# Optimization experiments

Measured on AMD Instinct MI355X. Metric: run time of the kernel, lower is better.

## Reference

```python
import jax, jax.numpy as jnp
import numpy as np


def channel_attention(x):
    # Faithful to torch: proj_key = x.view(B, -1, C) is a memory RESHAPE, not a transpose.
    B, C, H, W = x.shape
    N = H * W
    pq = x.reshape(B, C, N)          # [B, C, N]
    pk = x.reshape(B, N, C)          # [B, N, C] -- reshape, NOT pq transposed
    attn = jax.nn.softmax(jnp.einsum('bcn,bnd->bcd', pq, pk), axis=-1)  # [B, C, C]
    out = jnp.einsum('bcd,bdn->bcn', attn, pq).reshape(B, C, H, W)
    return out + x


def positional_attention(x):
    B, C, H, W = x.shape
    N = H * W
    pk = x.reshape(B, C, N)                                  # [B, C, N]
    # proj_query = pk transposed -> attn[b, n, m] over spatial positions
    attn = jax.nn.softmax(jnp.einsum('bcn,bcm->bnm', pk, pk), axis=-1)  # [B, N, N]
    # out = bmm(pk, attn^T): out[b, c, m] = sum_n pk[b, c, n] * attn[b, m, n]
    out = jnp.einsum('bcn,bmn->bcm', pk, attn).reshape(B, C, H, W)
    return out + x


def setup_inputs() -> dict:
    key = jax.random.key(0)
    x = jax.random.normal(key, (4, 512, 64, 64), dtype=jnp.float32)
    return {"x": x}


def reference(x):
    x_ca = channel_attention(x)
    x_pa = positional_attention(x_ca)
    return x_pa
```

## Files before the change

kernel.cpp:

```cpp
#include <hip/hip_runtime.h>

#define BATCH 4
#define CH 512
#define NSP 4096

typedef __attribute__((ext_vector_type(8))) short bfrag8;
typedef __attribute__((ext_vector_type(4))) float f32x4;
typedef unsigned short u16;

#define AS1 __attribute__((address_space(1)))
#define AS3 __attribute__((address_space(3)))
__device__ __forceinline__ void gload16(const void* g, void* l) {
    __builtin_amdgcn_global_load_lds((const AS1 void*)g, (AS3 void*)l, 16, 0, 0);
}

__device__ __forceinline__ void split_bf16(float y, u16& h, u16& l) {
    unsigned int u = __float_as_uint(y);
    h = (u16)(u >> 16);
    float r = y - __uint_as_float(((unsigned int)h) << 16);
    l = (u16)(__float_as_uint(r) >> 16);
}
__device__ __forceinline__ float join_bf16(u16 h, u16 l) {
    return __uint_as_float(((unsigned int)h) << 16) + __uint_as_float(((unsigned int)l) << 16);
}

__global__ __launch_bounds__(256) void k_prep_cn(const float* __restrict__ X,
                                                 u16* __restrict__ XHi,
                                                 u16* __restrict__ XLo,
                                                 u16* __restrict__ XT1hi,
                                                 u16* __restrict__ XT1lo) {
    __shared__ unsigned int t[64][65];
    const size_t boff = (size_t)blockIdx.z * CH * NSP;
    const int c0 = blockIdx.y * 64, n0 = blockIdx.x * 64;
    const int r = threadIdx.x >> 4, col4 = (threadIdx.x & 15) * 4;
#pragma unroll
    for (int it = 0; it < 4; it++) {
        int rl = r + it * 16;
        float4 v = *(const float4*)(X + boff + (size_t)(c0 + rl) * NSP + n0 + col4);
        ushort4 h, l;
        split_bf16(v.x, h.x, l.x);
        split_bf16(v.y, h.y, l.y);
        split_bf16(v.z, h.z, l.z);
        split_bf16(v.w, h.w, l.w);
        *(ushort4*)(XHi + boff + (size_t)(c0 + rl) * NSP + n0 + col4) = h;
        *(ushort4*)(XLo + boff + (size_t)(c0 + rl) * NSP + n0 + col4) = l;
        t[rl][col4 + 0] = ((unsigned int)h.x << 16) | l.x;
        t[rl][col4 + 1] = ((unsigned int)h.y << 16) | l.y;
        t[rl][col4 + 2] = ((unsigned int)h.z << 16) | l.z;
        t[rl][col4 + 3] = ((unsigned int)h.w << 16) | l.w;
    }
    __syncthreads();
#pragma unroll
    for (int it = 0; it < 4; it++) {
        int cl = r + it * 16;
        unsigned int p0 = t[col4 + 0][cl];
        unsigned int p1 = t[col4 + 1][cl];
        unsigned int p2 = t[col4 + 2][cl];
        unsigned int p3 = t[col4 + 3][cl];
        ushort4 hv, lv;
        hv.x = p0 >> 16; hv.y = p1 >> 16; hv.z = p2 >> 16; hv.w = p3 >> 16;
        lv.x = p0 & 0xffff; lv.y = p1 & 0xffff; lv.z = p2 & 0xffff; lv.w = p3 & 0xffff;
        *(ushort4*)(XT1hi + boff + (size_t)(n0 + cl) * CH + c0 + col4) = hv;
        *(ushort4*)(XT1lo + boff + (size_t)(n0 + cl) * CH + c0 + col4) = lv;
    }
}

__global__ __launch_bounds__(256) void k_prep_nc(const float* __restrict__ X,
                                                 u16* __restrict__ XT2hi,
                                                 u16* __restrict__ XT2lo) {
    __shared__ unsigned int t[64][65];
    const size_t boff = (size_t)blockIdx.z * CH * NSP;
    const int n0 = blockIdx.x * 64, d0 = blockIdx.y * 64;
    const int r = threadIdx.x >> 4, col4 = (threadIdx.x & 15) * 4;
#pragma unroll
    for (int it = 0; it < 4; it++) {
        int rl = r + it * 16;
        float4 v = *(const float4*)(X + boff + (size_t)(n0 + rl) * CH + d0 + col4);
        ushort4 h, l;
        split_bf16(v.x, h.x, l.x);
        split_bf16(v.y, h.y, l.y);
        split_bf16(v.z, h.z, l.z);
        split_bf16(v.w, h.w, l.w);
        t[rl][col4 + 0] = ((unsigned int)h.x << 16) | l.x;
        t[rl][col4 + 1] = ((unsigned int)h.y << 16) | l.y;
        t[rl][col4 + 2] = ((unsigned int)h.z << 16) | l.z;
        t[rl][col4 + 3] = ((unsigned int)h.w << 16) | l.w;
    }
    __syncthreads();
#pragma unroll
    for (int it = 0; it < 4; it++) {
        int cl = r + it * 16;
        unsigned int p0 = t[col4 + 0][cl];
        unsigned int p1 = t[col4 + 1][cl];
        unsigned int p2 = t[col4 + 2][cl];
        unsigned int p3 = t[col4 + 3][cl];
        ushort4 hv, lv;
        hv.x = p0 >> 16; hv.y = p1 >> 16; hv.z = p2 >> 16; hv.w = p3 >> 16;
        lv.x = p0 & 0xffff; lv.y = p1 & 0xffff; lv.z = p2 & 0xffff; lv.w = p3 & 0xffff;
        *(ushort4*)(XT2hi + boff + (size_t)(d0 + cl) * NSP + n0 + col4) = hv;
        *(ushort4*)(XT2lo + boff + (size_t)(d0 + cl) * NSP + n0 + col4) = lv;
    }
}

__global__ __launch_bounds__(256, 2) void k1_mfma(const u16* __restrict__ XHi,
                                                  const u16* __restrict__ XLo,
                                                  const u16* __restrict__ XT2hi,
                                                  const u16* __restrict__ XT2lo,
                                                  float* __restrict__ Pk) {
    __shared__ __align__(16) char smem[32768];
    char* Ahi = smem;
    char* Alo = smem + 8192;
    char* Bhi = smem + 16384;
    char* Blo = smem + 24576;
    const int bid = blockIdx.x;
    const int xcd = bid & 7;
    const int i1 = bid >> 3;
    const int group = xcd * 4 + (i1 >> 4);
    const int b = group >> 3, kz = group & 7;
    const int tile = i1 & 15;
    const int c0 = (tile >> 2) * 128, d0 = (tile & 3) * 128;
    const size_t boff = (size_t)b * CH * NSP;
    const int tid = threadIdx.x, lane = tid & 63, w = tid >> 6;
    const int wr = w >> 1, wc = w & 1;
    const int rl = lane >> 2;
    const int cb = (lane & 3) * 8;
    f32x4 acc[4][4];
#pragma unroll
    for (int i = 0; i < 4; i++)
#pragma unroll
        for (int j = 0; j < 4; j++) acc[i][j] = (f32x4){0.f, 0.f, 0.f, 0.f};

    const int kbeg = kz * 512, kend = kbeg + 512;
    for (int k0 = kbeg; k0 < kend; k0 += 32) {
#pragma unroll
        for (int s = 0; s < 2; s++) {
            int idx = w * 2 + s;
            int row = 16 * idx + rl;
            gload16(XHi + boff + (size_t)(c0 + row) * NSP + k0 + cb, Ahi + idx * 1024);
            gload16(XLo + boff + (size_t)(c0 + row) * NSP + k0 + cb, Alo + idx * 1024);
            gload16(XT2hi + boff + (size_t)(d0 + row) * NSP + k0 + cb, Bhi + idx * 1024);
            gload16(XT2lo + boff + (size_t)(d0 + row) * NSP + k0 + cb, Blo + idx * 1024);
        }
        __syncthreads();
        bfrag8 ah[4], al[4], bh[4], bl[4];
        const int q16 = (lane >> 4) * 16;
        const int l15 = (lane & 15);
#pragma unroll
        for (int i = 0; i < 4; i++) {
            int offa = (wr * 64 + i * 16 + l15) * 64 + q16;
            ah[i] = *(const bfrag8*)(Ahi + offa);
            al[i] = *(const bfrag8*)(Alo + offa);
            int offb = (wc * 64 + i * 16 + l15) * 64 + q16;
            bh[i] = *(const bfrag8*)(Bhi + offb);
            bl[i] = *(const bfrag8*)(Blo + offb);
        }
#pragma unroll
        for (int i = 0; i < 4; i++)
#pragma unroll
            for (int j = 0; j < 4; j++) {
                acc[i][j] = __builtin_amdgcn_mfma_f32_16x16x32_bf16(ah[i], bh[j], acc[i][j], 0, 0, 0);
                acc[i][j] = __builtin_amdgcn_mfma_f32_16x16x32_bf16(ah[i], bl[j], acc[i][j], 0, 0, 0);
                acc[i][j] = __builtin_amdgcn_mfma_f32_16x16x32_bf16(al[i], bh[j], acc[i][j], 0, 0, 0);
            }
        __syncthreads();
    }
    float* Lb = Pk + (size_t)kz * BATCH * CH * CH + (size_t)b * CH * CH;
    const int col = lane & 15, qr = (lane >> 4) * 4;
#pragma unroll
    for (int i = 0; i < 4; i++)
#pragma unroll
        for (int j = 0; j < 4; j++)
#pragma unroll
            for (int r = 0; r < 4; r++)
                Lb[(size_t)(c0 + wr * 64 + 16 * i + qr + r) * CH + d0 + wc * 64 + 16 * j + col] =
                    acc[i][j][r];
}

__global__ __launch_bounds__(256) void k_combine8(const float* __restrict__ Pk,
                                                  float* __restrict__ Lg) {
    const size_t MM = (size_t)BATCH * CH * CH;
    size_t i = ((size_t)blockIdx.x * 256 + threadIdx.x) * 4;
    float4 s = *(const float4*)(Pk + i);
#pragma unroll
    for (int z = 1; z < 8; z++) {
        float4 v = *(const float4*)(Pk + z * MM + i);
        s.x += v.x; s.y += v.y; s.z += v.z; s.w += v.w;
    }
    *(float4*)(Lg + i) = s;
}

__global__ __launch_bounds__(256) void k_softmax_pack512(float* __restrict__ Lg) {
    __shared__ float buf[512];
    __shared__ float red[256];
    const int tid = threadIdx.x;
    float* row = Lg + (size_t)blockIdx.x * 512;
    float2 v = *(const float2*)(row + tid * 2);
    buf[tid * 2] = v.x;
    buf[tid * 2 + 1] = v.y;
    red[tid] = fmaxf(v.x, v.y);
    __syncthreads();
    for (int s = 128; s > 0; s >>= 1) {
        if (tid < s) red[tid] = fmaxf(red[tid], red[tid + s]);
        __syncthreads();
    }
    float m = red[0];
    __syncthreads();
    float e0 = __expf(buf[tid * 2] - m), e1 = __expf(buf[tid * 2 + 1] - m);
    buf[tid * 2] = e0;
    buf[tid * 2 + 1] = e1;
    red[tid] = e0 + e1;
    __syncthreads();
    for (int s = 128; s > 0; s >>= 1) {
        if (tid < s) red[tid] += red[tid + s];
        __syncthreads();
    }
    float inv = 1.0f / red[0];
    u16* u = (u16*)row;
    u16 h0, l0, h1, l1;
    split_bf16(buf[tid * 2] * inv, h0, l0);
    split_bf16(buf[tid * 2 + 1] * inv, h1, l1);
    __syncthreads();
    u[tid * 2] = h0;
    u[tid * 2 + 1] = h1;
    u[512 + tid * 2] = l0;
    u[512 + tid * 2 + 1] = l1;
}

__global__ __launch_bounds__(256, 2) void k3_mfma(const u16* __restrict__ Lu,
                                                  const u16* __restrict__ XT1hi,
                                                  const u16* __restrict__ XT1lo,
                                                  const float* __restrict__ X,
                                                  u16* __restrict__ Yhi,
                                                  u16* __restrict__ Ylo,
                                                  u16* __restrict__ YThi,
                                                  u16* __restrict__ YTlo) {
    __shared__ __align__(16) char smem[33280];
    char* Ahi = smem;
    char* Alo = smem + 8192;
    char* Bhi = smem + 16384;
    char* Blo = smem + 24576;
    const int b = blockIdx.z;
    const u16* Au = Lu + (size_t)b * CH * 1024;
    const size_t boff = (size_t)b * CH * NSP;
    const float* Xb = X + boff;
    const int tid = threadIdx.x, lane = tid & 63, w = tid >> 6;
    const int wr = w >> 1, wc = w & 1;
    const int c0 = blockIdx.y * 128, n0 = blockIdx.x * 128;
    const int rl = lane >> 2;
    const int cb = (lane & 3) * 8;
    f32x4 acc[4][4];
#pragma unroll
    for (int i = 0; i < 4; i++)
#pragma unroll
        for (int j = 0; j < 4; j++) acc[i][j] = (f32x4){0.f, 0.f, 0.f, 0.f};

    for (int k0 = 0; k0 < CH; k0 += 32) {
#pragma unroll
        for (int s = 0; s < 2; s++) {
            int idx = w * 2 + s;
            int row = 16 * idx + rl;
            gload16(Au + (size_t)(c0 + row) * 1024 + k0 + cb, Ahi + idx * 1024);
            gload16(Au + (size_t)(c0 + row) * 1024 + 512 + k0 + cb, Alo + idx * 1024);
            gload16(XT1hi + boff + (size_t)(n0 + row) * CH + k0 + cb, Bhi + idx * 1024);
            gload16(XT1lo + boff + (size_t)(n0 + row) * CH + k0 + cb, Blo + idx * 1024);
        }
        __syncthreads();
        bfrag8 ah[4], al[4], bh[4], bl[4];
        const int q16 = (lane >> 4) * 16;
        const int l15 = (lane & 15);
#pragma unroll
        for (int i = 0; i < 4; i++) {
            int offa = (wr * 64 + i * 16 + l15) * 64 + q16;
            ah[i] = *(const bfrag8*)(Ahi + offa);
            al[i] = *(const bfrag8*)(Alo + offa);
            int offb = (wc * 64 + i * 16 + l15) * 64 + q16;
            bh[i] = *(const bfrag8*)(Bhi + offb);
            bl[i] = *(const bfrag8*)(Blo + offb);
        }
#pragma unroll
        for (int i = 0; i < 4; i++)
#pragma unroll
            for (int j = 0; j < 4; j++) {
                acc[i][j] = __builtin_amdgcn_mfma_f32_16x16x32_bf16(ah[i], bh[j], acc[i][j], 0, 0, 0);
                acc[i][j] = __builtin_amdgcn_mfma_f32_16x16x32_bf16(ah[i], bl[j], acc[i][j], 0, 0, 0);
                acc[i][j] = __builtin_amdgcn_mfma_f32_16x16x32_bf16(al[i], bh[j], acc[i][j], 0, 0, 0);
            }
        __syncthreads();
    }
    u16* Yhb = Yhi + boff;
    u16* Ylb = Ylo + boff;
    u16* YThb = YThi + boff;
    u16* YTlb = YTlo + boff;
    const int col = lane & 15, qr = (lane >> 4) * 4;
    unsigned int* Tb = (unsigned int*)smem;
#pragma unroll
    for (int round = 0; round < 2; round++) {
        if (wr == round) {
            unsigned int* T = Tb + wc * 4160;
#pragma unroll
            for (int i = 0; i < 4; i++)
#pragma unroll
                for (int j = 0; j < 4; j++)
#pragma unroll
                    for (int r = 0; r < 4; r++) {
                        int cl = 16 * i + qr + r;
                        int nl = 16 * j + col;
                        int c = c0 + wr * 64 + cl;
                        int n = n0 + wc * 64 + nl;
                        float v = acc[i][j][r] + Xb[(size_t)c * NSP + n];
                        u16 h, l;
                        split_bf16(v, h, l);
                        Yhb[(size_t)c * NSP + n] = h;
                        Ylb[(size_t)c * NSP + n] = l;
                        T[nl * 65 + cl] = ((unsigned int)h << 16) | l;
                    }
        }
        __syncthreads();
        if (wr == round) {
            unsigned int* T = Tb + wc * 4160;
            const int cl = (lane & 15) * 4;
#pragma unroll
            for (int rep = 0; rep < 16; rep++) {
                int nq = rep * 4 + (lane >> 4);
                unsigned int p0 = T[nq * 65 + cl];
                unsigned int p1 = T[nq * 65 + cl + 1];
                unsigned int p2 = T[nq * 65 + cl + 2];
                unsigned int p3 = T[nq * 65 + cl + 3];
                ushort4 hv, lv;
                hv.x = p0 >> 16; hv.y = p1 >> 16; hv.z = p2 >> 16; hv.w = p3 >> 16;
                lv.x = p0 & 0xffff; lv.y = p1 & 0xffff; lv.z = p2 & 0xffff; lv.w = p3 & 0xffff;
                size_t o = (size_t)(n0 + wc * 64 + nq) * CH + c0 + wr * 64 + cl;
                *(ushort4*)(YThb + o) = hv;
                *(ushort4*)(YTlb + o) = lv;
            }
        }
        __syncthreads();
    }
}

__global__ __launch_bounds__(512, 2) void k4_mfma(const u16* __restrict__ YThi0,
                                                  const u16* __restrict__ YTlo0,
                                                  float* __restrict__ S0) {
    __shared__ __align__(16) char smem[131072];
    const int tid = threadIdx.x, lane = tid & 63, w = tid >> 6;
    const int wr = w >> 2, wc = w & 3;
    const int bid = blockIdx.x;
    const int swz = (bid & 7) * 64 + (bid >> 3);
    const int rb = swz >> 8;
    const int tl = swz & 255;
    const int n0 = (tl >> 4) * 256, m0 = (tl & 15) * 256;
    const u16* Phi = YThi0 + (size_t)rb * NSP * CH;
    const u16* Plo = YTlo0 + (size_t)rb * NSP * CH;
    float* S = S0 + (size_t)rb * NSP * NSP;

    const int rl = lane >> 2;
    const int cb = (((lane & 3) ^ ((lane >> 3) & 3)) * 8);
    const int l15 = lane & 15;
    const int q16 = (((lane >> 4) ^ ((lane >> 1) & 3)) * 16);

    auto STAGE = [&](const u16* mat, int r0, int kt, int u) {
        char* dst = smem + (kt & 1) * 65536 + u * 16384;
        const int k0 = kt * 32;
#pragma unroll
        for (int s = 0; s < 2; s++) {
            int idx = w * 2 + s;
            gload16(mat + (size_t)(r0 + idx * 16 + rl) * CH + k0 + cb, dst + idx * 1024);
        }
    };

    f32x4 acc[8][4];
#pragma unroll
    for (int i = 0; i < 8; i++)
#pragma unroll
        for (int j = 0; j < 4; j++) acc[i][j] = (f32x4){0.f, 0.f, 0.f, 0.f};
    bfrag8 ah[8], al[8], bh[4], bl[4];

    auto LDA = [&](const char* base, bfrag8* a) {
#pragma unroll
        for (int i = 0; i < 8; i++)
            a[i] = *(const bfrag8*)(base + (wr * 128 + i * 16 + l15) * 64 + q16);
    };
    auto LDB = [&](const char* base, bfrag8* bv) {
#pragma unroll
        for (int j = 0; j < 4; j++)
            bv[j] = *(const bfrag8*)(base + (wc * 64 + j * 16 + l15) * 64 + q16);
    };
    auto MMA = [&](const bfrag8* a, const bfrag8* bv) {
        __builtin_amdgcn_s_setprio(1);
#pragma unroll
        for (int i = 0; i < 8; i++)
#pragma unroll
            for (int j = 0; j < 4; j++)
                acc[i][j] = __builtin_amdgcn_mfma_f32_16x16x32_bf16(a[i], bv[j], acc[i][j], 0, 0, 0);
        __builtin_amdgcn_s_setprio(0);
    };

#define WAITB(N)                                          \
    asm volatile("s_waitcnt vmcnt(" #N ")" ::: "memory"); \
    __builtin_amdgcn_sched_barrier(0);                    \
    __builtin_amdgcn_s_barrier();

    STAGE(Phi, n0, 0, 0);
    STAGE(Phi, m0, 0, 2);
    STAGE(Plo, n0, 0, 1);
    STAGE(Plo, m0, 0, 3);
    STAGE(Phi, n0, 1, 0);
    STAGE(Phi, m0, 1, 2);
    STAGE(Plo, n0, 1, 1);
    WAITB(10)

    for (int t = 0; t < 14; ++t) {
        const char* buf = smem + (t & 1) * 65536;
        LDA(buf, ah);
        LDB(buf + 32768, bh);
        STAGE(Plo, m0, t + 1, 3);
        WAITB(10)
        MMA(ah, bh);
        LDA(buf + 16384, al);
        STAGE(Phi, n0, t + 2, 0);
        STAGE(Phi, m0, t + 2, 2);
        WAITB(12)
        MMA(al, bh);
        LDB(buf + 49152, bl);
        STAGE(Plo, n0, t + 2, 1);
        WAITB(10)
        MMA(ah, bl);
    }
    {
        const char* buf = smem;
        LDA(buf, ah);
        LDB(buf + 32768, bh);
        STAGE(Plo, m0, 15, 3);
        WAITB(10)
        MMA(ah, bh);
        LDA(buf + 16384, al);
        WAITB(8)
        MMA(al, bh);
        LDB(buf + 49152, bl);
        WAITB(4)
        MMA(ah, bl);
    }
    {
        const char* buf = smem + 65536;
        LDA(buf, ah);
        LDB(buf + 32768, bh);
        WAITB(2)
        MMA(ah, bh);
        LDA(buf + 16384, al);
        WAITB(0)
        MMA(al, bh);
        LDB(buf + 49152, bl);
        MMA(ah, bl);
    }
#undef WAITB

    const int col = lane & 15, qr = (lane >> 4) * 4;
#pragma unroll
    for (int i = 0; i < 8; i++)
#pragma unroll
        for (int j = 0; j < 4; j++)
#pragma unroll
            for (int r = 0; r < 4; r++)
                S[(size_t)(n0 + wr * 128 + 16 * i + qr + r) * NSP + m0 + wc * 64 + 16 * j + col] =
                    acc[i][j][r];
}

__global__ __launch_bounds__(256) void k_softmax_pack(float* __restrict__ S) {
    __shared__ float buf[4096];
    __shared__ float red[256];
    const int tid = threadIdx.x;
    float* row = S + (size_t)blockIdx.x * NSP;
    float m = -INFINITY;
#pragma unroll
    for (int it = 0; it < 4; it++) {
        int i = (tid + it * 256) * 4;
        float4 v = *(const float4*)(row + i);
        buf[i] = v.x; buf[i + 1] = v.y; buf[i + 2] = v.z; buf[i + 3] = v.w;
        m = fmaxf(m, fmaxf(fmaxf(v.x, v.y), fmaxf(v.z, v.w)));
    }
    red[tid] = m;
    __syncthreads();
    for (int s = 128; s > 0; s >>= 1) {
        if (tid < s) red[tid] = fmaxf(red[tid], red[tid + s]);
        __syncthreads();
    }
    m = red[0];
    __syncthreads();
    float sum = 0.f;
#pragma unroll
    for (int it = 0; it < 4; it++) {
        int i = (tid + it * 256) * 4;
        float e0 = __expf(buf[i] - m), e1 = __expf(buf[i + 1] - m);
        float e2 = __expf(buf[i + 2] - m), e3 = __expf(buf[i + 3] - m);
        buf[i] = e0; buf[i + 1] = e1; buf[i + 2] = e2; buf[i + 3] = e3;
        sum += e0 + e1 + e2 + e3;
    }
    red[tid] = sum;
    __syncthreads();
    for (int s = 128; s > 0; s >>= 1) {
        if (tid < s) red[tid] += red[tid + s];
        __syncthreads();
    }
    float inv = 1.0f / red[0];
    u16* u = (u16*)row;
#pragma unroll
    for (int it = 0; it < 4; it++) {
        int i = (tid + it * 256) * 4;
        ushort4 hv;
        hv.x = (u16)(__float_as_uint(buf[i] * inv) >> 16);
        hv.y = (u16)(__float_as_uint(buf[i + 1] * inv) >> 16);
        hv.z = (u16)(__float_as_uint(buf[i + 2] * inv) >> 16);
        hv.w = (u16)(__float_as_uint(buf[i + 3] * inv) >> 16);
        *(ushort4*)(u + i) = hv;
    }
}

__global__ __launch_bounds__(512, 2) void k6_mfma(const u16* __restrict__ Yhi0,
                                                  const u16* __restrict__ Ylo0,
                                                  const u16* __restrict__ Su,
                                                  float* __restrict__ Out0,
                                                  float* __restrict__ Pp0,
                                                  float* __restrict__ Pp1) {
    __shared__ __align__(16) char smem[73728];
    const int tid = threadIdx.x, lane = tid & 63, w = tid >> 6;
    const int wr = w >> 2, wc = w & 3;
    const int m0 = blockIdx.x * 256, c0 = blockIdx.y * 128;
    const int rb = blockIdx.z >> 1, kz = blockIdx.z & 1;
    const u16* Yhi = Yhi0 + (size_t)rb * CH * NSP;
    const u16* Ylo = Ylo0 + (size_t)rb * CH * NSP;
    const u16* Pu = Su + (size_t)rb * NSP * NSP * 2;
    float* Out = Out0 + (size_t)rb * CH * NSP;
    float* Ppart = rb ? Pp1 : Pp0;
    const int kb = kz * 2048;
    const int rl = lane >> 2;
    const int cb = (((lane & 3) ^ ((lane >> 3) & 3)) * 8);
    const int l15 = lane & 15;
    const int q16 = (((lane >> 4) ^ ((lane >> 1) & 3)) * 16);

    auto STAGE = [&](int kt, int slot) {
        char* dst = smem + slot * 24576;
        const int k0 = kb + kt * 32;
        gload16(Yhi + (size_t)(c0 + w * 16 + rl) * NSP + k0 + cb, dst + w * 1024);
#pragma unroll
        for (int s = 0; s < 2; s++) {
            int idx = w * 2 + s;
            gload16(Pu + (size_t)(m0 + idx * 16 + rl) * 8192 + k0 + cb,
                    dst + 8192 + idx * 1024);
        }
    };

    f32x4 acc[4][4];
#pragma unroll
    for (int i = 0; i < 4; i++)
#pragma unroll
        for (int j = 0; j < 4; j++) acc[i][j] = (f32x4){0.f, 0.f, 0.f, 0.f};
    bfrag8 ah[4], bh[4];

#define K6PHASE(SLOT, STSLOT, T, DOSTAGE, WN)                                            \
    {                                                                                    \
        const char* bA = smem + (SLOT)*24576;                                            \
        const char* bB = bA + 8192;                                                      \
        _Pragma("unroll") for (int i = 0; i < 4; i++) ah[i] =                            \
            *(const bfrag8*)(bA + (wr * 64 + i * 16 + l15) * 64 + q16);                  \
        _Pragma("unroll") for (int j = 0; j < 4; j++) bh[j] =                            \
            *(const bfrag8*)(bB + (wc * 64 + j * 16 + l15) * 64 + q16);                  \
        if (DOSTAGE) STAGE((T) + 2, (STSLOT));                                           \
        asm volatile("s_waitcnt vmcnt(" #WN ")" ::: "memory");                           \
        __builtin_amdgcn_sched_barrier(0);                                               \
        __builtin_amdgcn_s_barrier();                                                    \
        __builtin_amdgcn_s_setprio(1);                                                   \
        _Pragma("unroll") for (int i = 0; i < 4; i++)                                    \
            _Pragma("unroll") for (int j = 0; j < 4; j++) acc[i][j] =                    \
                __builtin_amdgcn_mfma_f32_16x16x32_bf16(ah[i], bh[j], acc[i][j], 0, 0, 0); \
        __builtin_amdgcn_s_setprio(0);                                                   \
    }

    STAGE(0, 0);
    STAGE(1, 1);
    asm volatile("s_waitcnt vmcnt(3)" ::: "memory");
    __builtin_amdgcn_sched_barrier(0);
    __builtin_amdgcn_s_barrier();

    for (int tt = 0; tt < 60; tt += 3) {
        K6PHASE(0, 2, tt, true, 3)
        K6PHASE(1, 0, tt + 1, true, 3)
        K6PHASE(2, 1, tt + 2, true, 3)
    }
    K6PHASE(0, 2, 60, true, 3)
    K6PHASE(1, 0, 61, true, 3)
    K6PHASE(2, 0, 62, false, 0)
    K6PHASE(0, 0, 63, false, 0)
#undef K6PHASE

    const int col = lane & 15, qr = (lane >> 4) * 4;
    if (kz == 0) {
#pragma unroll
        for (int i = 0; i < 4; i++)
#pragma unroll
            for (int j = 0; j < 4; j++)
#pragma unroll
                for (int r = 0; r < 4; r++) {
                    int c = c0 + wr * 64 + 16 * i + qr + r;
                    int mm = m0 + wc * 64 + 16 * j + col;
                    Out[(size_t)c * NSP + mm] =
                        acc[i][j][r] +
                        join_bf16(Yhi[(size_t)c * NSP + mm], Ylo[(size_t)c * NSP + mm]);
                }
    } else {
#pragma unroll
        for (int i = 0; i < 4; i++)
#pragma unroll
            for (int j = 0; j < 4; j++)
#pragma unroll
                for (int r = 0; r < 4; r++) {
                    int c = c0 + wr * 64 + 16 * i + qr + r;
                    int mm = m0 + wc * 64 + 16 * j + col;
                    Ppart[(size_t)c * NSP + mm] = acc[i][j][r];
                }
    }
}

__global__ __launch_bounds__(256) void k_fixup(float* __restrict__ Out0,
                                               const float* __restrict__ Pp0,
                                               const float* __restrict__ Pp1) {
    const size_t CN = (size_t)CH * NSP;
    const int b = blockIdx.y;
    const float* P = b ? Pp1 : Pp0;
    float* O = Out0 + (size_t)b * CN;
    size_t i = ((size_t)blockIdx.x * 256 + threadIdx.x) * 4;
    float4 o = *(const float4*)(O + i);
    float4 a = *(const float4*)(P + i);
    o.x += a.x; o.y += a.y; o.z += a.z; o.w += a.w;
    *(float4*)(O + i) = o;
}

extern "C" void kernel_launch(void* const* d_in, const int* in_sizes, int n_in,
                              void* d_out, int out_size, void* d_ws, size_t ws_size,
                              hipStream_t stream) {
    const float* x = (const float*)d_in[0];
    float* out = (float*)d_out;

    char* p = (char*)d_ws;
    const size_t SZ16 = (size_t)BATCH * CH * NSP * 2;
    const size_t HALF = SZ16 / 2;
    u16* XHi = (u16*)p;
    u16* XLo = (u16*)(p + SZ16);
    u16* XT2hi = (u16*)(p + 2 * SZ16);
    u16* XT2lo = (u16*)(p + 3 * SZ16);
    u16* XT1hi = (u16*)(p + 4 * SZ16);
    u16* XT1lo = (u16*)(p + 5 * SZ16);
    float* S = (float*)p;
    u16* Yhi = (u16*)(p + 8 * SZ16);
    u16* Ylo = (u16*)(p + 9 * SZ16);
    u16* YThi = (u16*)(p + 10 * SZ16);
    u16* YTlo = (u16*)(p + 11 * SZ16);
    float* Pk = (float*)(p + 8 * SZ16);
    float* Lg = (float*)(p + 12 * SZ16);

    k_prep_cn<<<dim3(NSP / 64, CH / 64, BATCH), 256, 0, stream>>>(x, XHi, XLo, XT1hi, XT1lo);
    k_prep_nc<<<dim3(NSP / 64, CH / 64, BATCH), 256, 0, stream>>>(x, XT2hi, XT2lo);
    k1_mfma<<<dim3(512), 256, 0, stream>>>(XHi, XLo, XT2hi, XT2lo, Pk);
    k_combine8<<<dim3((BATCH * CH * CH) / (4 * 256)), 256, 0, stream>>>(Pk, Lg);
    k_softmax_pack512<<<dim3(BATCH * CH), 256, 0, stream>>>(Lg);
    k3_mfma<<<dim3(NSP / 128, CH / 128, BATCH), 256, 0, stream>>>((const u16*)Lg, XT1hi, XT1lo, x,
                                                                  Yhi, Ylo, YThi, YTlo);

    for (int round = 0; round < 2; round++) {
        const size_t b0 = (size_t)(2 * round);
        float* Pp0 = (float*)((char*)YThi + round * HALF);
        float* Pp1 = (float*)((char*)YTlo + round * HALF);
        k4_mfma<<<dim3(512), 512, 0, stream>>>(YThi + b0 * NSP * CH, YTlo + b0 * NSP * CH, S);
        k_softmax_pack<<<dim3(2 * NSP), 256, 0, stream>>>(S);
        k6_mfma<<<dim3(NSP / 256, CH / 128, 4), 512, 0, stream>>>(Yhi + b0 * CH * NSP,
                                                                  Ylo + b0 * CH * NSP,
                                                                  (const u16*)S,
                                                                  out + b0 * CH * NSP, Pp0, Pp1);
        k_fixup<<<dim3((CH * NSP) / (4 * 256), 2), 256, 0, stream>>>(out + b0 * CH * NSP, Pp0, Pp1);
    }
}
```

Baseline: 510.9 us.

## Prefetch next LDS fragments during MFMA blocks with register double-buffering

Restructures the main GEMM loop to double-buffer A/B register fragments and issue the next LDS reads right before each MFMA block, inside the high-priority region. The loop is unrolled by two so the two shared-memory buffers alternate explicitly. The intent is to hide LDS read latency behind matrix-core work. It costs extra VGPRs for the second fragment set, which may lower occupancy or cause spills. It also adds a barrier in the tail to keep the LDS reads ordered.

```diff
diff --git a/kernel.cpp b/kernel.cpp
--- a/kernel.cpp
+++ b/kernel.cpp
@@ -373,7 +373,7 @@
     for (int i = 0; i < 8; i++)
 #pragma unroll
         for (int j = 0; j < 4; j++) acc[i][j] = (f32x4){0.f, 0.f, 0.f, 0.f};
-    bfrag8 ah[8], al[8], bh[4], bl[4];
+    bfrag8 ah0[8], bh0[4], ah1[8], bh1[4], al[8], bl[4];
 
     auto LDA = [&](const char* base, bfrag8* a) {
 #pragma unroll
@@ -385,8 +385,9 @@
         for (int j = 0; j < 4; j++)
             bv[j] = *(const bfrag8*)(base + (wc * 64 + j * 16 + l15) * 64 + q16);
     };
-    auto MMA = [&](const bfrag8* a, const bfrag8* bv) {
+    auto MMAp = [&](const bfrag8* a, const bfrag8* bv, auto pre) {
         __builtin_amdgcn_s_setprio(1);
+        pre();
 #pragma unroll
         for (int i = 0; i < 8; i++)
 #pragma unroll
@@ -399,6 +400,9 @@
     asm volatile("s_waitcnt vmcnt(" #N ")" ::: "memory"); \
     __builtin_amdgcn_sched_barrier(0);                    \
     __builtin_amdgcn_s_barrier();
+
+    const char* b0 = smem;
+    const char* b1 = smem + 65536;
 
     STAGE(Phi, n0, 0, 0);
     STAGE(Phi, m0, 0, 2);
@@ -408,49 +412,57 @@
     STAGE(Phi, m0, 1, 2);
     STAGE(Plo, n0, 1, 1);
     WAITB(10)
-
-    for (int t = 0; t < 14; ++t) {
-        const char* buf = smem + (t & 1) * 65536;
-        LDA(buf, ah);
-        LDB(buf + 32768, bh);
+    LDA(b0, ah0);
+    LDB(b0 + 32768, bh0);
+
+    for (int t = 0; t < 14; t += 2) {
         STAGE(Plo, m0, t + 1, 3);
         WAITB(10)
-        MMA(ah, bh);
-        LDA(buf + 16384, al);
+        MMAp(ah0, bh0, [&] { LDA(b0 + 16384, al); });
         STAGE(Phi, n0, t + 2, 0);
         STAGE(Phi, m0, t + 2, 2);
         WAITB(12)
-        MMA(al, bh);
-        LDB(buf + 49152, bl);
+        MMAp(al, bh0, [&] { LDB(b0 + 49152, bl); });
         STAGE(Plo, n0, t + 2, 1);
         WAITB(10)
-        MMA(ah, bl);
+        MMAp(ah0, bl, [&] {
+            LDA(b1, ah1);
+            LDB(b1 + 32768, bh1);
+        });
+        STAGE(Plo, m0, t + 2, 3);
+        WAITB(10)
+        MMAp(ah1, bh1, [&] { LDA(b1 + 16384, al); });
+        STAGE(Phi, n0, t + 3, 0);
+        STAGE(Phi, m0, t + 3, 2);
+        WAITB(12)
+        MMAp(al, bh1, [&] { LDB(b1 + 49152, bl); });
+        STAGE(Plo, n0, t + 3, 1);
+        WAITB(10)
+        MMAp(ah1, bl, [&] {
+            LDA(b0, ah0);
+            LDB(b0 + 32768, bh0);
+        });
     }
     {
-        const char* buf = smem;
-        LDA(buf, ah);
-        LDB(buf + 32768, bh);
         STAGE(Plo, m0, 15, 3);
         WAITB(10)
-        MMA(ah, bh);
-        LDA(buf + 16384, al);
+        MMAp(ah0, bh0, [&] { LDA(b0 + 16384, al); });
         WAITB(8)
-        MMA(al, bh);
-        LDB(buf + 49152, bl);
+        MMAp(al, bh0, [&] { LDB(b0 + 49152, bl); });
         WAITB(4)
-        MMA(ah, bl);
+        MMAp(ah0, bl, [&] {
+            LDA(b1, ah1);
+            LDB(b1 + 32768, bh1);
+        });
     }
     {
-        const char* buf = smem + 65536;
-        LDA(buf, ah);
-        LDB(buf + 32768, bh);
         WAITB(2)
-        MMA(ah, bh);
-        LDA(buf + 16384, al);
+        MMAp(ah1, bh1, [&] { LDA(b1 + 16384, al); });
         WAITB(0)
-        MMA(al, bh);
-        LDB(buf + 49152, bl);
-        MMA(ah, bl);
+        MMAp(al, bh1, [&] { LDB(b1 + 49152, bl); });
+        __builtin_amdgcn_sched_barrier(0);
+        __builtin_amdgcn_s_barrier();
+        MMAp(ah1, bl, [&] {});
     }
 #undef WAITB
 
```

Result: slower. 554.9 us (+8.6%).

## Exploit symmetry of positional Gram matrix by computing only lower-triangular tiles

Applied to the files above, without the earlier changes.

The positional attention logits S = Y^T Y are symmetric, so k4 now launches only the lower-triangular 128x128 tiles and writes each off-diagonal tile a second time, transposed, through LDS. This roughly halves the MFMA work and operand loads for the largest GEMM. In exchange the tiles shrink from 256x256 with 8 waves to 128x128 with 4 waves, which lowers per-block reuse. It also adds an extra transposed store pass with LDS round trips and a per-block triangular index decode.

```diff
diff --git a/kernel.cpp b/kernel.cpp
--- a/kernel.cpp
+++ b/kernel.cpp
@@ -338,20 +338,23 @@
     }
 }
 
-__global__ __launch_bounds__(512, 2) void k4_mfma(const u16* __restrict__ YThi0,
+__global__ __launch_bounds__(256, 2) void k4_mfma(const u16* __restrict__ YThi0,
                                                   const u16* __restrict__ YTlo0,
                                                   float* __restrict__ S0) {
-    __shared__ __align__(16) char smem[131072];
+    __shared__ __align__(16) char smem[65536];
     const int tid = threadIdx.x, lane = tid & 63, w = tid >> 6;
-    const int wr = w >> 2, wc = w & 3;
-    const int bid = blockIdx.x;
-    const int swz = (bid & 7) * 64 + (bid >> 3);
-    const int rb = swz >> 8;
-    const int tl = swz & 255;
-    const int n0 = (tl >> 4) * 256, m0 = (tl & 15) * 256;
+    const int wr = w >> 1, wc = w & 1;
+    const int rb = blockIdx.y;
     const u16* Phi = YThi0 + (size_t)rb * NSP * CH;
     const u16* Plo = YTlo0 + (size_t)rb * NSP * CH;
     float* S = S0 + (size_t)rb * NSP * NSP;
+    int idx = blockIdx.x;
+    int bi = (int)((sqrtf(8.f * (float)idx + 1.f) - 1.f) * 0.5f);
+    while ((bi + 1) * (bi + 2) / 2 <= idx) bi++;
+    while (bi * (bi + 1) / 2 > idx) bi--;
+    int bj = idx - bi * (bi + 1) / 2;
+    const int n0 = bi * 128, m0 = bj * 128;
+    const bool diag = (bi == bj);
 
     const int rl = lane >> 2;
     const int cb = (((lane & 3) ^ ((lane >> 3) & 3)) * 8);
@@ -359,26 +362,26 @@
     const int q16 = (((lane >> 4) ^ ((lane >> 1) & 3)) * 16);
 
     auto STAGE = [&](const u16* mat, int r0, int kt, int u) {
-        char* dst = smem + (kt & 1) * 65536 + u * 16384;
+        char* dst = smem + (kt & 1) * 32768 + u * 8192;
         const int k0 = kt * 32;
 #pragma unroll
         for (int s = 0; s < 2; s++) {
-            int idx = w * 2 + s;
-            gload16(mat + (size_t)(r0 + idx * 16 + rl) * CH + k0 + cb, dst + idx * 1024);
+            int i2 = w * 2 + s;
+            gload16(mat + (size_t)(r0 + i2 * 16 + rl) * CH + k0 + cb, dst + i2 * 1024);
         }
     };
 
-    f32x4 acc[8][4];
-#pragma unroll
-    for (int i = 0; i < 8; i++)
+    f32x4 acc[4][4];
+#pragma unroll
+    for (int i = 0; i < 4; i++)
 #pragma unroll
         for (int j = 0; j < 4; j++) acc[i][j] = (f32x4){0.f, 0.f, 0.f, 0.f};
-    bfrag8 ah[8], al[8], bh[4], bl[4];
+    bfrag8 ah[4], al[4], bh[4], bl[4];
 
     auto LDA = [&](const char* base, bfrag8* a) {
 #pragma unroll
-        for (int i = 0; i < 8; i++)
-            a[i] = *(const bfrag8*)(base + (wr * 128 + i * 16 + l15) * 64 + q16);
+        for (int i = 0; i < 4; i++)
+            a[i] = *(const bfrag8*)(base + (wr * 64 + i * 16 + l15) * 64 + q16);
     };
     auto LDB = [&](const char* base, bfrag8* bv) {
 #pragma unroll
@@ -388,7 +391,7 @@
     auto MMA = [&](const bfrag8* a, const bfrag8* bv) {
         __builtin_amdgcn_s_setprio(1);
 #pragma unroll
-        for (int i = 0; i < 8; i++)
+        for (int i = 0; i < 4; i++)
 #pragma unroll
             for (int j = 0; j < 4; j++)
                 acc[i][j] = __builtin_amdgcn_mfma_f32_16x16x32_bf16(a[i], bv[j], acc[i][j], 0, 0, 0);
@@ -410,18 +413,18 @@
     WAITB(10)
 
     for (int t = 0; t < 14; ++t) {
-        const char* buf = smem + (t & 1) * 65536;
+        const char* buf = smem + (t & 1) * 32768;
         LDA(buf, ah);
-        LDB(buf + 32768, bh);
+        LDB(buf + 16384, bh);
         STAGE(Plo, m0, t + 1, 3);
         WAITB(10)
         MMA(ah, bh);
-        LDA(buf + 16384, al);
+        LDA(buf + 8192, al);
         STAGE(Phi, n0, t + 2, 0);
         STAGE(Phi, m0, t + 2, 2);
         WAITB(12)
         MMA(al, bh);
-        LDB(buf + 49152, bl);
+        LDB(buf + 24576, bl);
         STAGE(Plo, n0, t + 2, 1);
         WAITB(10)
         MMA(ah, bl);
@@ -429,40 +432,70 @@
     {
         const char* buf = smem;
         LDA(buf, ah);
-        LDB(buf + 32768, bh);
+        LDB(buf + 16384, bh);
         STAGE(Plo, m0, 15, 3);
         WAITB(10)
         MMA(ah, bh);
-        LDA(buf + 16384, al);
+        LDA(buf + 8192, al);
         WAITB(8)
         MMA(al, bh);
-        LDB(buf + 49152, bl);
+        LDB(buf + 24576, bl);
         WAITB(4)
         MMA(ah, bl);
     }
     {
-        const char* buf = smem + 65536;
+        const char* buf = smem + 32768;
         LDA(buf, ah);
-        LDB(buf + 32768, bh);
+        LDB(buf + 16384, bh);
         WAITB(2)
         MMA(ah, bh);
-        LDA(buf + 16384, al);
+        LDA(buf + 8192, al);
         WAITB(0)
         MMA(al, bh);
-        LDB(buf + 49152, bl);
+        LDB(buf + 24576, bl);
+        __builtin_amdgcn_sched_barrier(0);
+        __builtin_amdgcn_s_barrier();
         MMA(ah, bl);
     }
 #undef WAITB
 
     const int col = lane & 15, qr = (lane >> 4) * 4;
 #pragma unroll
-    for (int i = 0; i < 8; i++)
+    for (int i = 0; i < 4; i++)
 #pragma unroll
         for (int j = 0; j < 4; j++)
 #pragma unroll
             for (int r = 0; r < 4; r++)
-                S[(size_t)(n0 + wr * 128 + 16 * i + qr + r) * NSP + m0 + wc * 64 + 16 * j + col] =
+                S[(size_t)(n0 + wr * 64 + 16 * i + qr + r) * NSP + m0 + wc * 64 + 16 * j + col] =
                     acc[i][j][r];
+    if (!diag) {
+        float* Tbase = (float*)smem;
+#pragma unroll
+        for (int round = 0; round < 2; round++) {
+            __syncthreads();
+            if (wr == round) {
+                float* T = Tbase + wc * (64 * 68);
+#pragma unroll
+                for (int i = 0; i < 4; i++)
+#pragma unroll
+                    for (int j = 0; j < 4; j++)
+#pragma unroll
+                        for (int r = 0; r < 4; r++)
+                            T[(16 * j + col) * 68 + 16 * i + qr + r] = acc[i][j][r];
+            }
+            __syncthreads();
+            if (wr == round) {
+                float* T = Tbase + wc * (64 * 68);
+                const int rq = (lane & 15) * 4;
+#pragma unroll
+                for (int rep = 0; rep < 16; rep++) {
+                    int cq = rep * 4 + (lane >> 4);
+                    float4 v = *(const float4*)(T + cq * 68 + rq);
+                    *(float4*)(S + (size_t)(m0 + wc * 64 + cq) * NSP + n0 + wr * 64 + rq) = v;
+                }
+            }
+        }
+    }
 }
 
 __global__ __launch_bounds__(256) void k_softmax_pack(float* __restrict__ S) {
@@ -665,11 +698,12 @@
     k3_mfma<<<dim3(NSP / 128, CH / 128, BATCH), 256, 0, stream>>>((const u16*)Lg, XT1hi, XT1lo, x,
                                                                   Yhi, Ylo, YThi, YTlo);
 
+    const int TRI = (NSP / 128) * (NSP / 128 + 1) / 2;
     for (int round = 0; round < 2; round++) {
         const size_t b0 = (size_t)(2 * round);
         float* Pp0 = (float*)((char*)YThi + round * HALF);
         float* Pp1 = (float*)((char*)YTlo + round * HALF);
-        k4_mfma<<<dim3(512), 512, 0, stream>>>(YThi + b0 * NSP * CH, YTlo + b0 * NSP * CH, S);
+        k4_mfma<<<dim3(TRI, 2), 256, 0, stream>>>(YThi + b0 * NSP * CH, YTlo + b0 * NSP * CH, S);
         k_softmax_pack<<<dim3(2 * NSP), 256, 0, stream>>>(S);
         k6_mfma<<<dim3(NSP / 256, CH / 128, 4), 512, 0, stream>>>(Yhi + b0 * CH * NSP,
                                                                   Ylo + b0 * CH * NSP,
```

Result: faster. 466.0 us (-8.8%).
